# Kernel optimization log

Hardware: AMD Instinct MI355X
Metric: run time of the kernel (lower is better)

The kernel has to match this reference:

```python
import jax, jax.numpy as jnp
import numpy as np

N = 40000          # nodes
E = 1280000        # edges (avg degree 32)
S = 64             # num_scalars
V = 16             # num_vectors
R = 32             # num_radial
CUTOFF = 10.0


def setup_inputs() -> dict:
    key = jax.random.key(0)
    ks = jax.random.split(key, 12)
    scalars = jax.random.normal(ks[0], (N, S), dtype=jnp.float32)
    vectors = jax.random.normal(ks[1], (N, V, 3), dtype=jnp.float32)
    edge_index = jax.random.randint(ks[2], (2, E), 0, N, dtype=jnp.int64)
    edge_vec = jax.random.normal(ks[3], (E, 3), dtype=jnp.float32)
    # radial_net: Linear(R,R) -> SiLU -> Linear(R, S + 2V)
    W1 = jax.random.normal(ks[4], (R, R), dtype=jnp.float32) * 0.1
    b1 = jnp.zeros((R,), dtype=jnp.float32)
    W2 = jax.random.normal(ks[5], (R, S + 2 * V), dtype=jnp.float32) * 0.1
    b2 = jnp.zeros((S + 2 * V,), dtype=jnp.float32)
    # attention: Linear(2S+R, S) -> SiLU -> Linear(S, 1)
    Wa1 = jax.random.normal(ks[6], (2 * S + R, S), dtype=jnp.float32) * 0.1
    ba1 = jnp.zeros((S,), dtype=jnp.float32)
    Wa2 = jax.random.normal(ks[7], (S, 1), dtype=jnp.float32) * 0.1
    ba2 = jnp.zeros((1,), dtype=jnp.float32)
    return dict(scalars=scalars, vectors=vectors, edge_vec=edge_vec,
                W1=W1, b1=b1, W2=W2, b2=b2,
                Wa1=Wa1, ba1=ba1, Wa2=Wa2, ba2=ba2,
                edge_index=edge_index)


def reference(scalars, vectors, edge_vec, W1, b1, W2, b2, Wa1, ba1, Wa2, ba2, edge_index):
    src = edge_index[0]  # j (source)
    dst = edge_index[1]  # i (target / aggregation index)

    d = jnp.linalg.norm(edge_vec, axis=-1)                 # [E]
    d_safe = jnp.clip(d[:, None], 1e-8, None)              # [E,1]

    # Bessel radial basis with cosine cutoff
    freqs = (jnp.arange(1, R + 1, dtype=jnp.float32) * np.pi / CUTOFF)
    bessel = jnp.sin(freqs * d[:, None]) / d_safe          # [E,R]
    cut = 0.5 * (jnp.cos(np.pi * d[:, None] / CUTOFF) + 1.0)
    cut = cut * (d[:, None] < CUTOFF).astype(jnp.float32)
    rbf = bessel * cut                                     # [E,R]

    # spherical harmonics (lmax=1); vector already normalized, sh = [1, y, z, x]
    unit = edge_vec / d_safe                               # [E,3]
    sh_weight = jnp.stack([unit[:, 1], unit[:, 2], unit[:, 0]], axis=-1)  # [E,3]

    # radial filter MLP
    filters = jax.nn.silu(rbf @ W1 + b1) @ W2 + b2         # [E, S+2V]
    scalar_filter = filters[:, :S]
    vector_filter = filters[:, S:S + V]
    vector_gate = filters[:, S + V:]

    s_i = scalars[dst]                                     # [E,S]
    s_j = scalars[src]                                     # [E,S]
    v_j = vectors[src]                                     # [E,V,3]

    scalar_message = s_j * scalar_filter                   # [E,S]
    vector_message = (v_j * vector_filter[:, :, None]
                      + vector_gate[:, :, None] * sh_weight[:, None, :])  # [E,V,3]

    att_in = jnp.concatenate([s_i, s_j, rbf], axis=-1)     # [E, 2S+R]
    att = jax.nn.sigmoid(jax.nn.silu(att_in @ Wa1 + ba1) @ Wa2 + ba2)  # [E,1]

    scalar_message = att * scalar_message
    vector_message = att[:, :, None] * vector_message

    scalar_aggr = jax.ops.segment_sum(scalar_message, dst, num_segments=N)
    vector_aggr = jax.ops.segment_sum(vector_message, dst, num_segments=N)

    return scalars + scalar_aggr, vectors + vector_aggr
```

## Files before the change

kernel.cpp:

```cpp
#include <hip/hip_runtime.h>

static constexpr int N_ = 40000;
static constexpr int E_ = 1280000;
static constexpr int NS = N_ * 64;
static constexpr int NV = N_ * 48;

typedef _Float16 half2_t __attribute__((ext_vector_type(2)));
typedef _Float16 half8_t __attribute__((ext_vector_type(8)));
typedef float float4_t __attribute__((ext_vector_type(4)));
typedef unsigned int uint;

__device__ __forceinline__ float silu_f(float x) { return __fdividef(x, 1.f + __expf(-x)); }
__device__ __forceinline__ int rfl(int x) { return __builtin_amdgcn_readfirstlane(x); }

static constexpr int PATT_BLOCKS = 512;
__global__ __launch_bounds__(256) void k_patt(
    const float* __restrict__ scalars, const float* __restrict__ Wa1,
    const float* __restrict__ ba1,
    _Float16* __restrict__ P1h, _Float16* __restrict__ P2h)
{
    int gw   = (blockIdx.x * 256 + threadIdx.x) >> 6;
    int lane = threadIdx.x & 63;
    float w[128];
#pragma unroll
    for (int k = 0; k < 128; k++) w[k] = Wa1[k * 64 + lane];
    float bias = ba1[lane];
    for (int n = gw; n < N_; n += PATT_BLOCKS * 4) {
        float sv = scalars[(size_t)n * 64 + lane];
        float a1 = bias, a2 = 0.f;
#pragma unroll
        for (int k = 0; k < 64; k++) {
            float sk = __shfl(sv, k, 64);
            a1 = fmaf(sk, w[k], a1);
            a2 = fmaf(sk, w[64 + k], a2);
        }
        P1h[(size_t)n * 64 + lane] = (_Float16)a1;
        P2h[(size_t)n * 64 + lane] = (_Float16)a2;
    }
}

__global__ void k_convp(const float* __restrict__ scalars, const float* __restrict__ vectors,
                        _Float16* __restrict__ sc16p, _Float16* __restrict__ vec16p,
                        const float* __restrict__ W1, const float* __restrict__ Wa1,
                        const float* __restrict__ W2, uint* __restrict__ tbl,
                        uint* __restrict__ tbl2)
{
    if (blockIdx.x >= 5000) {
        int t = (blockIdx.x - 5000) * 256 + threadIdx.x;
        if (t < 1536) {
            int j = t >> 4, q = t & 15;
            int k0 = 2 * q, k1 = 2 * q + 1;
            float a = (j < 64) ? Wa1[(128 + k0) * 64 + j] : W1[k0 * 32 + (j - 64)];
            float b = (j < 64) ? Wa1[(128 + k1) * 64 + j] : W1[k1 * 32 + (j - 64)];
            half2_t v; v.x = (_Float16)a; v.y = (_Float16)b;
            tbl[t] = __builtin_bit_cast(uint, v);
        } else if (t < 3072) {
            int tt = t - 1536;
            int j = tt >> 4, q = tt & 15;
            half2_t v;
            v.x = (_Float16)W2[(2 * q + 0) * 96 + j];
            v.y = (_Float16)W2[(2 * q + 1) * 96 + j];
            tbl2[tt] = __builtin_bit_cast(uint, v);
        }
        return;
    }
    int t = blockIdx.x * 256 + threadIdx.x;
    if (t < N_ * 16) {
        int n = t >> 4, bl = t & 15;
        const float* srow = scalars + (size_t)n * 64;
        half2_t a, b;
        a.x = (_Float16)srow[bl];
        a.y = (_Float16)srow[16 + bl];
        b.x = (_Float16)srow[32 + bl];
        b.y = (_Float16)srow[48 + bl];
        uint2 u; u.x = __builtin_bit_cast(uint, a); u.y = __builtin_bit_cast(uint, b);
        *(uint2*)(sc16p + (size_t)n * 64 + bl * 4) = u;
    } else {
        int tt = t - N_ * 16;
        int n = tt >> 4, bl = tt & 15;
        const float* vrow = vectors + (size_t)n * 48 + bl * 3;
        half2_t a, b;
        a.x = (_Float16)vrow[0];
        a.y = (_Float16)vrow[1];
        b.x = (_Float16)vrow[2];
        b.y = (_Float16)0.f;
        uint2 u; u.x = __builtin_bit_cast(uint, a); u.y = __builtin_bit_cast(uint, b);
        *(uint2*)(vec16p + (size_t)n * 64 + bl * 4) = u;
    }
}

__global__ void k_rank(const int* __restrict__ eidx, int* __restrict__ cnt,
                       int* __restrict__ r)
{
    int e = blockIdx.x * 256 + threadIdx.x;
    r[e] = atomicAdd(&cnt[eidx[E_ + e]], 1);
}

__global__ void k_scan1(const int* __restrict__ cnt, int* __restrict__ row_start,
                        int* __restrict__ bsum)
{
    __shared__ int buf[1024];
    int b = blockIdx.x, tid = threadIdx.x;
    int idx = b * 1024 + tid;
    int v = (idx < N_) ? cnt[idx] : 0;
    buf[tid] = v;
    __syncthreads();
    for (int off = 1; off < 1024; off <<= 1) {
        int t = (tid >= off) ? buf[tid - off] : 0;
        __syncthreads();
        buf[tid] += t;
        __syncthreads();
    }
    if (idx < N_) row_start[idx] = buf[tid] - v;
    if (tid == 1023) bsum[b] = buf[1023];
}

__global__ void k_scan3(const int* __restrict__ bsum, int* __restrict__ row_start)
{
    __shared__ int boffs;
    if (threadIdx.x == 0) {
        int s = 0;
        for (int b = 0; b < (int)blockIdx.x; b++) s += bsum[b];
        boffs = s;
    }
    __syncthreads();
    int idx = blockIdx.x * 1024 + threadIdx.x;
    if (idx < N_) row_start[idx] += boffs;
    if (idx == N_) row_start[N_] = E_;
}

__global__ void k_place2(const int* __restrict__ eidx, const float* __restrict__ edge_vec,
                         const int* __restrict__ row_start, const int* __restrict__ r,
                         float4* __restrict__ evs, int* __restrict__ srcs,
                         int* __restrict__ dsts)
{
    int e = blockIdx.x * 256 + threadIdx.x;
    int src = eidx[e];
    int dst = eidx[E_ + e];
    int slot = row_start[dst] + r[e];
    evs[slot] = make_float4(edge_vec[3 * e + 0], edge_vec[3 * e + 1], edge_vec[3 * e + 2], 0.f);
    srcs[slot] = src;
    dsts[slot] = dst;
}

__global__ __launch_bounds__(256, 3) void k_edges_sorted(
    const float4* __restrict__ evs, const int* __restrict__ srcs,
    const int* __restrict__ dsts,
    const _Float16* __restrict__ P1h, const _Float16* __restrict__ P2h,
    const uint* __restrict__ tbl, const float* __restrict__ b1,
    const float* __restrict__ Wa2, const float* __restrict__ ba2,
    float4* __restrict__ attsh, uint* __restrict__ hbufp)
{
    __shared__ char lds_raw[4 * 12544];
    int tid = threadIdx.x;
    int wid = tid >> 6, lane = tid & 63;
    char* wbase = lds_raw + wid * 12544;
    int bl = lane & 15, bq = lane >> 4;

    int i = blockIdx.x * 256 + tid;
    float4 ev4 = evs[i];
    int src = srcs[i];
    int dst = dsts[i];

    float ev0 = ev4.x, ev1 = ev4.y, ev2 = ev4.z;
    float d = sqrtf(fmaf(ev0, ev0, fmaf(ev1, ev1, ev2 * ev2)));
    float inv_d = __fdividef(1.f, fmaxf(d, 1e-8f));
    float cut = (d < 10.f) ? 0.5f * (__cosf(0.31415927f * d) + 1.f) : 0.f;
    float cutd = cut * inv_d;
    float sh0 = ev1 * inv_d, sh1 = ev2 * inv_d, sh2 = ev0 * inv_d;

    float th = 0.31415927f * d;
    float scur = __sinf(th);
    float twoC = 2.f * __cosf(th);
    float sprev = 0.f;
    uint rbf2[16];
#pragma unroll
    for (int q = 0; q < 16; q++) {
        float r0 = scur * cutd;
        float snext = fmaf(twoC, scur, -sprev);
        sprev = scur; scur = snext;
        float r1 = scur * cutd;
        snext = fmaf(twoC, scur, -sprev);
        sprev = scur; scur = snext;
        half2_t v; v.x = (_Float16)r0; v.y = (_Float16)r1;
        rbf2[q] = __builtin_bit_cast(uint, v);
    }
    {
        uint4* rw = (uint4*)(wbase + lane * 64);
        rw[0] = make_uint4(rbf2[0], rbf2[1], rbf2[2], rbf2[3]);
        rw[1] = make_uint4(rbf2[4], rbf2[5], rbf2[6], rbf2[7]);
        rw[2] = make_uint4(rbf2[8], rbf2[9], rbf2[10], rbf2[11]);
        rw[3] = make_uint4(rbf2[12], rbf2[13], rbf2[14], rbf2[15]);
    }
    uint4 bfr[6];
#pragma unroll
    for (int u = 0; u < 6; u++)
        bfr[u] = *(const uint4*)(tbl + (u * 16 + bl) * 16 + bq * 4);

    uint4 afr[4];
#pragma unroll
    for (int t = 0; t < 4; t++)
        afr[t] = *(const uint4*)(wbase + (t * 16 + bl) * 64 + bq * 16);

    _Float16* gtile = (_Float16*)wbase;
#pragma unroll
    for (int t = 0; t < 4; t++) {
        half8_t av = __builtin_bit_cast(half8_t, afr[t]);
        int eb = t * 16 + bq * 4;
#pragma unroll
        for (int u = 0; u < 6; u++) {
            float4_t dd = __builtin_amdgcn_mfma_f32_16x16x32_f16(
                av, __builtin_bit_cast(half8_t, bfr[u]), (float4_t)(0.f), 0, 0, 0);
            int col = u * 16 + bl;
            gtile[(eb + 0) * 98 + col] = (_Float16)dd[0];
            gtile[(eb + 1) * 98 + col] = (_Float16)dd[1];
            gtile[(eb + 2) * 98 + col] = (_Float16)dd[2];
            gtile[(eb + 3) * 98 + col] = (_Float16)dd[3];
        }
    }
    const uint* grow = (const uint*)(wbase + (size_t)lane * 196);

    const uint2* p1h = (const uint2*)(P1h + (size_t)dst * 64);
    const uint2* p2h = (const uint2*)(P2h + (size_t)src * 64);
    float logit = ba2[0];
#pragma unroll
    for (int q = 0; q < 16; q++) {
        uint2 ua = p1h[q];
        uint2 ub = p2h[q];
        half2_t s01 = __builtin_bit_cast(half2_t, ua.x) + __builtin_bit_cast(half2_t, ub.x)
                    + __builtin_bit_cast(half2_t, grow[2 * q + 0]);
        half2_t s23 = __builtin_bit_cast(half2_t, ua.y) + __builtin_bit_cast(half2_t, ub.y)
                    + __builtin_bit_cast(half2_t, grow[2 * q + 1]);
        logit = fmaf(silu_f((float)s01.x), Wa2[4 * q + 0], logit);
        logit = fmaf(silu_f((float)s01.y), Wa2[4 * q + 1], logit);
        logit = fmaf(silu_f((float)s23.x), Wa2[4 * q + 2], logit);
        logit = fmaf(silu_f((float)s23.y), Wa2[4 * q + 3], logit);
    }
    float att = __fdividef(1.f, 1.f + __expf(-logit));

    uint hp[16];
#pragma unroll
    for (int q = 0; q < 16; q++) {
        half2_t gg = __builtin_bit_cast(half2_t, grow[32 + q]);
        half2_t v;
        v.x = (_Float16)silu_f((float)gg.x + b1[2 * q + 0]);
        v.y = (_Float16)silu_f((float)gg.y + b1[2 * q + 1]);
        hp[q] = __builtin_bit_cast(uint, v);
    }
    uint4* hrow4 = (uint4*)(hbufp + (size_t)i * 16);
#pragma unroll
    for (int q = 0; q < 4; q++)
        hrow4[q] = make_uint4(hp[4 * q + 0], hp[4 * q + 1], hp[4 * q + 2], hp[4 * q + 3]);
    attsh[i] = make_float4(att, sh0, sh1, sh2);
}

__global__ __launch_bounds__(256, 4) void k_gather_mfma(
    const float* __restrict__ scalars, const float* __restrict__ vectors,
    const _Float16* __restrict__ sc16p, const _Float16* __restrict__ vec16p,
    const float* __restrict__ b2,
    const int* __restrict__ row_start,
    const float4* __restrict__ attsh, const int* __restrict__ srcbuf,
    const uint* __restrict__ hbuf, const uint* __restrict__ tbl2,
    float* __restrict__ out)
{
    int wid  = threadIdx.x >> 6;
    int lane = threadIdx.x & 63;
    int n    = blockIdx.x * 4 + wid;
    int bl = lane & 15, bq = lane >> 4;
    int rs = rfl(row_start[n]);
    int re = rfl(row_start[n + 1]);

    uint4 bfr2[6];
#pragma unroll
    for (int u = 0; u < 6; u++)
        bfr2[u] = *(const uint4*)(tbl2 + (u * 16 + bl) * 16 + bq * 4);

    float b2s[4];
#pragma unroll
    for (int u = 0; u < 4; u++) b2s[u] = b2[u * 16 + bl];
    float bvf = b2[64 + bl], bvg = b2[80 + bl];

    float accS0 = 0.f, accS1 = 0.f, accS2 = 0.f, accS3 = 0.f;
    float accV0 = 0.f, accV1 = 0.f, accV2 = 0.f;

    for (int i0 = rs; i0 < re; i0 += 16) {
        uint4 av4 = make_uint4(0u, 0u, 0u, 0u);
        if (i0 + bl < re)
            av4 = *(const uint4*)(hbuf + (size_t)(i0 + bl) * 16 + bq * 4);
        half8_t av = __builtin_bit_cast(half8_t, av4);

        float4_t d0 = __builtin_amdgcn_mfma_f32_16x16x32_f16(av, __builtin_bit_cast(half8_t, bfr2[0]), (float4_t)(0.f), 0, 0, 0);
        float4_t d1 = __builtin_amdgcn_mfma_f32_16x16x32_f16(av, __builtin_bit_cast(half8_t, bfr2[1]), (float4_t)(0.f), 0, 0, 0);
        float4_t d2 = __builtin_amdgcn_mfma_f32_16x16x32_f16(av, __builtin_bit_cast(half8_t, bfr2[2]), (float4_t)(0.f), 0, 0, 0);
        float4_t d3 = __builtin_amdgcn_mfma_f32_16x16x32_f16(av, __builtin_bit_cast(half8_t, bfr2[3]), (float4_t)(0.f), 0, 0, 0);
        float4_t d4 = __builtin_amdgcn_mfma_f32_16x16x32_f16(av, __builtin_bit_cast(half8_t, bfr2[4]), (float4_t)(0.f), 0, 0, 0);
        float4_t d5 = __builtin_amdgcn_mfma_f32_16x16x32_f16(av, __builtin_bit_cast(half8_t, bfr2[5]), (float4_t)(0.f), 0, 0, 0);

#pragma unroll
        for (int r = 0; r < 4; r++) {
            int slot = i0 + bq * 4 + r;
            int ok = (slot < re);
            int cs = ok ? slot : (re - 1);
            float4 as = attsh[cs];
            float att = ok ? as.x : 0.f;
            int src = srcbuf[cs];
            uint2 su = *(const uint2*)(sc16p + (size_t)src * 64 + bl * 4);
            uint2 vu = *(const uint2*)(vec16p + (size_t)src * 64 + bl * 4);
            half2_t s01 = __builtin_bit_cast(half2_t, su.x);
            half2_t s23 = __builtin_bit_cast(half2_t, su.y);
            half2_t v01 = __builtin_bit_cast(half2_t, vu.x);
            half2_t v23 = __builtin_bit_cast(half2_t, vu.y);
            accS0 = fmaf(att * (float)s01.x, d0[r] + b2s[0], accS0);
            accS1 = fmaf(att * (float)s01.y, d1[r] + b2s[1], accS1);
            accS2 = fmaf(att * (float)s23.x, d2[r] + b2s[2], accS2);
            accS3 = fmaf(att * (float)s23.y, d3[r] + b2s[3], accS3);
            float vf = d4[r] + bvf;
            float vg = d5[r] + bvg;
            accV0 = fmaf(att, fmaf((float)v01.x, vf, vg * as.y), accV0);
            accV1 = fmaf(att, fmaf((float)v01.y, vf, vg * as.z), accV1);
            accV2 = fmaf(att, fmaf((float)v23.x, vf, vg * as.w), accV2);
        }
    }

    accS0 += __shfl_xor(accS0, 16, 64); accS0 += __shfl_xor(accS0, 32, 64);
    accS1 += __shfl_xor(accS1, 16, 64); accS1 += __shfl_xor(accS1, 32, 64);
    accS2 += __shfl_xor(accS2, 16, 64); accS2 += __shfl_xor(accS2, 32, 64);
    accS3 += __shfl_xor(accS3, 16, 64); accS3 += __shfl_xor(accS3, 32, 64);
    accV0 += __shfl_xor(accV0, 16, 64); accV0 += __shfl_xor(accV0, 32, 64);
    accV1 += __shfl_xor(accV1, 16, 64); accV1 += __shfl_xor(accV1, 32, 64);
    accV2 += __shfl_xor(accV2, 16, 64); accV2 += __shfl_xor(accV2, 32, 64);

    if (bq == 0) {
        size_t o = (size_t)n * 64 + bl;
        out[o +  0] = scalars[o +  0] + accS0;
        out[o + 16] = scalars[o + 16] + accS1;
        out[o + 32] = scalars[o + 32] + accS2;
        out[o + 48] = scalars[o + 48] + accS3;
        size_t ov = (size_t)n * 48 + 3 * bl;
        out[NS + ov + 0] = vectors[ov + 0] + accV0;
        out[NS + ov + 1] = vectors[ov + 1] + accV1;
        out[NS + ov + 2] = vectors[ov + 2] + accV2;
    }
}

extern "C" void kernel_launch(void* const* d_in, const int* in_sizes, int n_in,
                              void* d_out, int out_size, void* d_ws, size_t ws_size,
                              hipStream_t stream)
{
    const float* scalars  = (const float*)d_in[0];
    const float* vectors  = (const float*)d_in[1];
    const float* edge_vec = (const float*)d_in[2];
    const float* W1  = (const float*)d_in[3];
    const float* b1  = (const float*)d_in[4];
    const float* W2  = (const float*)d_in[5];
    const float* b2  = (const float*)d_in[6];
    const float* Wa1 = (const float*)d_in[7];
    const float* ba1 = (const float*)d_in[8];
    const float* Wa2 = (const float*)d_in[9];
    const float* ba2 = (const float*)d_in[10];
    const int* eidx  = (const int*)d_in[11];

    char* wsb = (char*)d_ws;
    float4* attsh = (float4*)wsb;
    float*  P1    = (float*)(wsb + (size_t)E_ * 16);
    float*  P2    = P1 + NS;
    float*  hbuf  = P2 + NS;
    int* cnt       = (int*)(hbuf + (size_t)32 * E_);
    int* bsum      = cnt + N_;
    int* boff      = bsum + 64;
    int* row_start = cnt + 2 * N_;
    int* perm      = row_start + N_ + 1;
    int* srcbuf    = perm + E_;
    int*  rnk  = (int*)hbuf;
    uint* tbl  = (uint*)hbuf + (size_t)16 * E_;
    uint* tbl2 = tbl + 1536;
    _Float16* P1h  = (_Float16*)(tbl2 + 1536);
    _Float16* P2h  = P1h + NS;
    _Float16* sc16p = P2h + NS;
    _Float16* vec16p = (_Float16*)P1;
    float4* evs = (float4*)(sc16p + NS);
    int* dsts   = (int*)(evs + E_);

    hipMemsetAsync(cnt, 0, (size_t)N_ * sizeof(int), stream);
    k_rank<<<5000, 256, 0, stream>>>(eidx, cnt, rnk);
    k_scan1<<<40, 1024, 0, stream>>>(cnt, row_start, bsum);
    k_scan3<<<40, 1024, 0, stream>>>(bsum, row_start);
    k_place2<<<5000, 256, 0, stream>>>(eidx, edge_vec, row_start, rnk, evs, srcbuf, dsts);
    k_patt<<<PATT_BLOCKS, 256, 0, stream>>>(scalars, Wa1, ba1, P1h, P2h);
    k_convp<<<5012, 256, 0, stream>>>(scalars, vectors, sc16p, vec16p, W1, Wa1, W2, tbl, tbl2);
    k_edges_sorted<<<5000, 256, 0, stream>>>(evs, srcbuf, dsts, P1h, P2h,
                                             tbl, b1, Wa2, ba2,
                                             attsh, (uint*)hbuf);
    k_gather_mfma<<<10000, 256, 0, stream>>>(scalars, vectors, sc16p, vec16p, b2, row_start,
                                             attsh, srcbuf, (const uint*)hbuf, tbl2,
                                             (float*)d_out);
}
```

Baseline: 404.6 us.

## Fuse edge placement into edge kernel and pack att, sh and src per slot

Removes the k_place2 scatter kernel. The edge kernel now reads edges in original order and computes each edge's sorted slot from row_start and rank, then scatters its hidden activations and a 32-byte metadata row (att, sh, src) straight to that slot. The gather kernel reads the src index from the same metadata row instead of a separate srcbuf. This saves one launch and the write and reread of the sorted edge_vec, src and dst arrays. In exchange, the edge kernel's stores become scattered, its P1h/P2h gathers follow random dst order instead of sorted order, and the metadata row grows from 16 to 32 bytes.

New measurement: 415.5 us. 2.7% more time.

```diff
diff --git a/kernel.cpp b/kernel.cpp
--- a/kernel.cpp
+++ b/kernel.cpp
@@ -129,27 +129,13 @@
     if (idx == N_) row_start[N_] = E_;
 }
 
-__global__ void k_place2(const int* __restrict__ eidx, const float* __restrict__ edge_vec,
-                         const int* __restrict__ row_start, const int* __restrict__ r,
-                         float4* __restrict__ evs, int* __restrict__ srcs,
-                         int* __restrict__ dsts)
-{
-    int e = blockIdx.x * 256 + threadIdx.x;
-    int src = eidx[e];
-    int dst = eidx[E_ + e];
-    int slot = row_start[dst] + r[e];
-    evs[slot] = make_float4(edge_vec[3 * e + 0], edge_vec[3 * e + 1], edge_vec[3 * e + 2], 0.f);
-    srcs[slot] = src;
-    dsts[slot] = dst;
-}
-
-__global__ __launch_bounds__(256, 3) void k_edges_sorted(
-    const float4* __restrict__ evs, const int* __restrict__ srcs,
-    const int* __restrict__ dsts,
+__global__ __launch_bounds__(256, 3) void k_edges_fused(
+    const float* __restrict__ edge_vec, const int* __restrict__ eidx,
+    const int* __restrict__ rnk, const int* __restrict__ row_start,
     const _Float16* __restrict__ P1h, const _Float16* __restrict__ P2h,
     const uint* __restrict__ tbl, const float* __restrict__ b1,
     const float* __restrict__ Wa2, const float* __restrict__ ba2,
-    float4* __restrict__ attsh, uint* __restrict__ hbufp)
+    float* __restrict__ metap, uint* __restrict__ hbufp)
 {
     __shared__ char lds_raw[4 * 12544];
     int tid = threadIdx.x;
@@ -157,12 +143,14 @@
     char* wbase = lds_raw + wid * 12544;
     int bl = lane & 15, bq = lane >> 4;
 
-    int i = blockIdx.x * 256 + tid;
-    float4 ev4 = evs[i];
-    int src = srcs[i];
-    int dst = dsts[i];
-
-    float ev0 = ev4.x, ev1 = ev4.y, ev2 = ev4.z;
+    int e = blockIdx.x * 256 + tid;
+    int src = eidx[e];
+    int dst = eidx[E_ + e];
+    int slot = row_start[dst] + rnk[e];
+
+    float ev0 = edge_vec[3 * e + 0];
+    float ev1 = edge_vec[3 * e + 1];
+    float ev2 = edge_vec[3 * e + 2];
     float d = sqrtf(fmaf(ev0, ev0, fmaf(ev1, ev1, ev2 * ev2)));
     float inv_d = __fdividef(1.f, fmaxf(d, 1e-8f));
     float cut = (d < 10.f) ? 0.5f * (__cosf(0.31415927f * d) + 1.f) : 0.f;
@@ -247,11 +235,13 @@
         v.y = (_Float16)silu_f((float)gg.y + b1[2 * q + 1]);
         hp[q] = __builtin_bit_cast(uint, v);
     }
-    uint4* hrow4 = (uint4*)(hbufp + (size_t)i * 16);
+    uint4* hrow4 = (uint4*)(hbufp + (size_t)slot * 16);
 #pragma unroll
     for (int q = 0; q < 4; q++)
         hrow4[q] = make_uint4(hp[4 * q + 0], hp[4 * q + 1], hp[4 * q + 2], hp[4 * q + 3]);
-    attsh[i] = make_float4(att, sh0, sh1, sh2);
+    float* mrow = metap + (size_t)slot * 8;
+    *(float4*)(mrow)     = make_float4(att, sh0, sh1, sh2);
+    *(float4*)(mrow + 4) = make_float4(__int_as_float(src), 0.f, 0.f, 0.f);
 }
 
 __global__ __launch_bounds__(256, 4) void k_gather_mfma(
@@ -259,7 +249,7 @@
     const _Float16* __restrict__ sc16p, const _Float16* __restrict__ vec16p,
     const float* __restrict__ b2,
     const int* __restrict__ row_start,
-    const float4* __restrict__ attsh, const int* __restrict__ srcbuf,
+    const float* __restrict__ metap,
     const uint* __restrict__ hbuf, const uint* __restrict__ tbl2,
     float* __restrict__ out)
 {
@@ -301,9 +291,10 @@
             int slot = i0 + bq * 4 + r;
             int ok = (slot < re);
             int cs = ok ? slot : (re - 1);
-            float4 as = attsh[cs];
+            const float* mrow = metap + (size_t)cs * 8;
+            float4 as = *(const float4*)(mrow);
+            int src = __float_as_int(mrow[4]);
             float att = ok ? as.x : 0.f;
-            int src = srcbuf[cs];
             uint2 su = *(const uint2*)(sc16p + (size_t)src * 64 + bl * 4);
             uint2 vu = *(const uint2*)(vec16p + (size_t)src * 64 + bl * 4);
             half2_t s01 = __builtin_bit_cast(half2_t, su.x);
@@ -361,37 +352,29 @@
     const int* eidx  = (const int*)d_in[11];
 
     char* wsb = (char*)d_ws;
-    float4* attsh = (float4*)wsb;
-    float*  P1    = (float*)(wsb + (size_t)E_ * 16);
-    float*  P2    = P1 + NS;
-    float*  hbuf  = P2 + NS;
+    float* metap = (float*)wsb;
+    float* hbuf  = (float*)(wsb + (size_t)E_ * 32);
     int* cnt       = (int*)(hbuf + (size_t)32 * E_);
     int* bsum      = cnt + N_;
-    int* boff      = bsum + 64;
     int* row_start = cnt + 2 * N_;
-    int* perm      = row_start + N_ + 1;
-    int* srcbuf    = perm + E_;
-    int*  rnk  = (int*)hbuf;
+    int* rnk       = row_start + N_ + 1;
     uint* tbl  = (uint*)hbuf + (size_t)16 * E_;
     uint* tbl2 = tbl + 1536;
     _Float16* P1h  = (_Float16*)(tbl2 + 1536);
     _Float16* P2h  = P1h + NS;
     _Float16* sc16p = P2h + NS;
-    _Float16* vec16p = (_Float16*)P1;
-    float4* evs = (float4*)(sc16p + NS);
-    int* dsts   = (int*)(evs + E_);
+    _Float16* vec16p = sc16p + NS;
 
     hipMemsetAsync(cnt, 0, (size_t)N_ * sizeof(int), stream);
     k_rank<<<5000, 256, 0, stream>>>(eidx, cnt, rnk);
     k_scan1<<<40, 1024, 0, stream>>>(cnt, row_start, bsum);
     k_scan3<<<40, 1024, 0, stream>>>(bsum, row_start);
-    k_place2<<<5000, 256, 0, stream>>>(eidx, edge_vec, row_start, rnk, evs, srcbuf, dsts);
     k_patt<<<PATT_BLOCKS, 256, 0, stream>>>(scalars, Wa1, ba1, P1h, P2h);
     k_convp<<<5012, 256, 0, stream>>>(scalars, vectors, sc16p, vec16p, W1, Wa1, W2, tbl, tbl2);
-    k_edges_sorted<<<5000, 256, 0, stream>>>(evs, srcbuf, dsts, P1h, P2h,
-                                             tbl, b1, Wa2, ba2,
-                                             attsh, (uint*)hbuf);
+    k_edges_fused<<<5000, 256, 0, stream>>>(edge_vec, eidx, rnk, row_start, P1h, P2h,
+                                            tbl, b1, Wa2, ba2,
+                                            metap, (uint*)hbuf);
     k_gather_mfma<<<10000, 256, 0, stream>>>(scalars, vectors, sc16p, vec16p, b2, row_start,
-                                             attsh, srcbuf, (const uint*)hbuf, tbl2,
+                                             metap, (const uint*)hbuf, tbl2,
                                              (float*)d_out);
 }
```
